# Kernel tuning notes

Measured on AMD Instinct MI355X. Metric: run time of the kernel, lower is better.

The kernel has to match this reference:

```python
import jax, jax.numpy as jnp
import numpy as np

HIDDEN = 1024
NUM_HEADS = 16
HEAD_DIM = HIDDEN // NUM_HEADS


def setup_inputs() -> dict:
    key = jax.random.key(0)
    k1, k2, k3 = jax.random.split(key, 3)
    x = jax.random.normal(k1, (2, 2048, HIDDEN), dtype=jnp.float32)
    # Linear weights, torch layout [out_features, in_features]
    w_qkv = jax.random.normal(k2, (3 * HIDDEN, HIDDEN), dtype=jnp.float32) * 0.02
    w_out = jax.random.normal(k3, (HIDDEN, HIDDEN), dtype=jnp.float32) * 0.02
    return {"x": x, "w_qkv": w_qkv, "w_out": w_out}


def reference(x, w_qkv, w_out):
    B, S, H = x.shape
    scale = 1.0 / HEAD_DIM ** 0.5
    qkv = jnp.einsum('bsh,oh->bso', x, w_qkv)              # [B,S,3H]
    qkv = qkv.reshape(B, S, 3, NUM_HEADS, HEAD_DIM)
    qkv = jnp.transpose(qkv, (2, 0, 3, 1, 4))               # [3,B,nh,S,hd]
    q, k, v = qkv[0], qkv[1], qkv[2]
    scores = jnp.einsum('bnsd,bntd->bnst', q, k) * scale    # [B,nh,S,S]
    attn = jax.nn.softmax(scores, axis=-1)
    out = jnp.einsum('bnst,bntd->bnsd', attn, v)            # [B,nh,S,hd]
    out = jnp.transpose(out, (0, 2, 1, 3)).reshape(B, S, H)
    return jnp.einsum('bsh,oh->bso', out, w_out)
```

## Files before the change

### kernel.cpp

```cpp
#include <hip/hip_runtime.h>
#include <stdint.h>

typedef unsigned short u16;
typedef __bf16 bf16x8 __attribute__((ext_vector_type(8)));
typedef float f32x4 __attribute__((ext_vector_type(4)));
typedef float f32x16 __attribute__((ext_vector_type(16)));
typedef unsigned u32x4 __attribute__((ext_vector_type(4)));

#define DEVI __device__ __forceinline__

typedef __attribute__((address_space(1))) void gvoid;
typedef __attribute__((address_space(3))) void lvoid;

DEVI u16 f2b(float f) {
  unsigned x = __builtin_bit_cast(unsigned, f);
  return (u16)((x + 0x7fffu + ((x >> 16) & 1u)) >> 16);
}

DEVI float exp2g(float x) { return __builtin_amdgcn_exp2f(x); }

DEVI void gload_lds16(const void* g, void* l) {
  __builtin_amdgcn_global_load_lds((gvoid*)g, (lvoid*)l, 16, 0, 0);
}

#define QSCALE 0.18033688011112042f

__global__ void cast_all(const float* __restrict__ x, const float* __restrict__ wqkv,
                         const float* __restrict__ wout, u16* __restrict__ outb) {
  int i = blockIdx.x * 256 + threadIdx.x;
  int stride = gridDim.x * 256;
  for (; i < 2097152; i += stride) {
    const float* src;
    float sc = 1.0f;
    if (i < 1048576) {
      src = x + 4 * (long)i;
    } else if (i < 1835008) {
      int j = i - 1048576;
      src = wqkv + 4 * (long)j;
      if (j < 262144) sc = QSCALE;
    } else {
      src = wout + 4 * (long)(i - 1835008);
    }
    float4 v = *(const float4*)src;
    ushort4 o;
    o.x = f2b(v.x * sc); o.y = f2b(v.y * sc); o.z = f2b(v.z * sc); o.w = f2b(v.w * sc);
    ((ushort4*)outb)[i] = o;
  }
}

__global__ __launch_bounds__(512, 2)
void gemm_qkv(const u16* __restrict__ A, const u16* __restrict__ B,
              u16* __restrict__ qk, u16* __restrict__ vT, int K) {
  __shared__ u16 SA[2][256 * 64];
  __shared__ u16 SB[2][256 * 64];
  const int tid = threadIdx.x;
  const int lane = tid & 63;
  const int lr = lane & 15;
  const int lg = lane >> 4;
  const int wid = tid >> 6;
  const int wm = wid >> 2;
  const int wn = wid & 3;
  const long bm = (long)blockIdx.y * 256;
  const long bn = (long)blockIdx.x * 256;
  const int wr = wm * 128;
  const int wc = wn * 64;

  f32x4 acc[8][4];
#pragma unroll
  for (int i = 0; i < 8; ++i)
#pragma unroll
    for (int j = 0; j < 4; ++j)
      acc[i][j] = (f32x4){0.f, 0.f, 0.f, 0.f};

  int srow[4], scol[4], sdst[4];
#pragma unroll
  for (int q = 0; q < 4; ++q) {
    int b = tid + q * 512;
    srow[q] = b >> 3;
    scol[q] = ((b & 7) ^ ((b >> 3) & 7)) * 8;
    sdst[q] = b * 16;
  }

  auto stage = [&](int buf, int k0) {
#pragma unroll
    for (int q = 0; q < 4; ++q)
      gload_lds16(A + (bm + srow[q]) * (long)K + k0 + scol[q], (char*)SA[buf] + sdst[q]);
#pragma unroll
    for (int q = 0; q < 4; ++q)
      gload_lds16(B + (bn + srow[q]) * (long)K + k0 + scol[q], (char*)SB[buf] + sdst[q]);
  };

  stage(0, 0);
  asm volatile("s_waitcnt vmcnt(0)" ::: "memory");
  __builtin_amdgcn_s_barrier();
  __builtin_amdgcn_sched_barrier(0);

  const int NITER = K >> 6;
  for (int it = 0; it < NITER; ++it) {
    const int cur = it & 1;
    if (it + 1 < NITER) stage(cur ^ 1, (it + 1) * 64);

    const char* cA = (const char*)SA[cur];
    const char* cB = (const char*)SB[cur];

    bf16x8 bf[4][2];
#pragma unroll
    for (int ni = 0; ni < 4; ++ni)
#pragma unroll
      for (int kk = 0; kk < 2; ++kk) {
        int row = wc + ni * 16 + lr;
        bf[ni][kk] = *(const bf16x8*)(cB + row * 128 + (((kk * 4 + lg) ^ (row & 7)) << 4));
      }

#pragma unroll
    for (int half = 0; half < 2; ++half) {
      bf16x8 af[4][2];
#pragma unroll
      for (int mi = 0; mi < 4; ++mi)
#pragma unroll
        for (int kk = 0; kk < 2; ++kk) {
          int row = wr + half * 64 + mi * 16 + lr;
          af[mi][kk] = *(const bf16x8*)(cA + row * 128 + (((kk * 4 + lg) ^ (row & 7)) << 4));
        }
      __builtin_amdgcn_s_setprio(1);
#pragma unroll
      for (int mi = 0; mi < 4; ++mi)
#pragma unroll
        for (int ni = 0; ni < 4; ++ni)
#pragma unroll
          for (int kk = 0; kk < 2; ++kk)
            acc[half * 4 + mi][ni] =
                __builtin_amdgcn_mfma_f32_16x16x32_bf16(af[mi][kk], bf[ni][kk], acc[half * 4 + mi][ni], 0, 0, 0);
      __builtin_amdgcn_s_setprio(0);
    }

    if (it + 1 < NITER) {
      asm volatile("s_waitcnt vmcnt(0)" ::: "memory");
      __builtin_amdgcn_s_barrier();
      __builtin_amdgcn_sched_barrier(0);
    }
  }

  if (bn >= 2048) {
#pragma unroll
    for (int mi = 0; mi < 8; ++mi)
#pragma unroll
      for (int ni = 0; ni < 4; ++ni) {
        long tok = bm + wr + mi * 16 + lg * 4;
        long f = bn + wc + ni * 16 + lr - 2048;
        ushort4 st;
        st.x = f2b(acc[mi][ni][0]);
        st.y = f2b(acc[mi][ni][1]);
        st.z = f2b(acc[mi][ni][2]);
        st.w = f2b(acc[mi][ni][3]);
        u16* dst = vT + (((tok >> 11) << 4) + (f >> 6)) * 131072 + (f & 63) * 2048 + (tok & 2047);
        *(ushort4*)dst = st;
      }
  } else {
#pragma unroll
    for (int mi = 0; mi < 8; ++mi)
#pragma unroll
      for (int ni = 0; ni < 4; ++ni)
#pragma unroll
        for (int r = 0; r < 4; ++r) {
          long row = bm + wr + mi * 16 + lg * 4 + r;
          long col = bn + wc + ni * 16 + lr;
          qk[row * 2048 + col] = f2b(acc[mi][ni][r]);
        }
  }
}

template<int OUT, int TM, int SWZ>
__global__ __launch_bounds__(256)
void gemm_bt(const u16* __restrict__ A, const u16* __restrict__ B, void* __restrict__ Cv,
             void* __restrict__ Cv2, int M, int N, int K) {
  constexpr int MI = TM / 32;
  __shared__ u16 lA[TM * 64];
  __shared__ u16 lB[128 * 64];
  const int tid = threadIdx.x;
  const int lane = tid & 63;
  const int lr = lane & 15;
  const int lg = lane >> 4;
  const int wid = tid >> 6;

  long bm, bn;
  if (SWZ) {
    const int f = blockIdx.x + gridDim.x * blockIdx.y;
    const int chunk = (gridDim.x * gridDim.y) >> 3;
    const int ln = (f & 7) * chunk + (f >> 3);
    bm = (long)(ln % gridDim.y) * TM;
    bn = (long)(ln / gridDim.y) * 128;
  } else {
    bm = (long)blockIdx.y * TM;
    bn = (long)blockIdx.x * 128;
  }

  const int wr = (wid >> 1) * (TM / 2);
  const int wc = (wid & 1) * 64;

  f32x4 acc[MI][4];
#pragma unroll
  for (int i = 0; i < MI; ++i)
#pragma unroll
    for (int j = 0; j < 4; ++j)
      acc[i][j] = (f32x4){0.f, 0.f, 0.f, 0.f};

  for (int k0 = 0; k0 < K; k0 += 64) {
#pragma unroll
    for (int q = 0; q < MI; ++q) {
      int bi = tid + q * 256;
      int row = bi >> 3;
      int col = ((bi & 7) ^ (row & 7)) * 8;
      gload_lds16(A + (bm + row) * (long)K + k0 + col, (char*)lA + bi * 16);
    }
#pragma unroll
    for (int q = 0; q < 4; ++q) {
      int bi = tid + q * 256;
      int row = bi >> 3;
      int col = ((bi & 7) ^ (row & 7)) * 8;
      gload_lds16(B + (bn + row) * (long)K + k0 + col, (char*)lB + bi * 16);
    }
    __syncthreads();
#pragma unroll
    for (int kk = 0; kk < 2; ++kk) {
      bf16x8 af[MI], bfr[4];
      int kb = kk * 4 + lg;
#pragma unroll
      for (int mi = 0; mi < MI; ++mi) {
        int row = wr + mi * 16 + lr;
        af[mi] = *(const bf16x8*)((const char*)lA + row * 128 + ((kb ^ (row & 7)) << 4));
      }
#pragma unroll
      for (int ni = 0; ni < 4; ++ni) {
        int row = wc + ni * 16 + lr;
        bfr[ni] = *(const bf16x8*)((const char*)lB + row * 128 + ((kb ^ (row & 7)) << 4));
      }
#pragma unroll
      for (int mi = 0; mi < MI; ++mi)
#pragma unroll
        for (int ni = 0; ni < 4; ++ni)
          acc[mi][ni] = __builtin_amdgcn_mfma_f32_16x16x32_bf16(af[mi], bfr[ni], acc[mi][ni], 0, 0, 0);
    }
    __syncthreads();
  }

  const long strideN = (OUT == 2) ? 2048 : N;
#pragma unroll
  for (int mi = 0; mi < MI; ++mi)
#pragma unroll
    for (int ni = 0; ni < 4; ++ni)
#pragma unroll
      for (int r = 0; r < 4; ++r) {
        long row = bm + wr + mi * 16 + lg * 4 + r;
        long col = bn + wc + ni * 16 + lr;
        float v = acc[mi][ni][r];
        if (OUT == 1) ((float*)Cv)[row * strideN + col] = v;
        else          ((u16*)Cv)[row * strideN + col] = f2b(v);
      }
}

__global__ __launch_bounds__(256, 2)
void attn_fwd(const u16* __restrict__ qk, const u16* __restrict__ vT,
              u16* __restrict__ outb) {
  __shared__ char SM[33280];

  const int tid = threadIdx.x;
  const int lane = tid & 63;
  const int wid = tid >> 6;
  const int ql = lane & 31;
  const int h  = lane >> 5;
  const int th = wid >> 1;
  const int qw = wid & 1;

  const int flat = blockIdx.x + (blockIdx.y << 4) + (blockIdx.z << 8);
  const int swz  = ((flat & 7) << 6) + (flat >> 3);
  const int qt = swz & 15;
  const int hd = (swz >> 4) & 15;
  const int b  = swz >> 8;

  const long rowbase = (long)b * 2048;
  const int qcol = hd * 64;
  const int kcol = 1024 + hd * 64;
  const int TSK = 64 * 2048;
  const long vhb = ((long)b * 16 + hd) * 131072;

  const int q0w = qt * 128 + qw * 64;
  bf16x8 qfA[4], qfB[4];
  {
    const u16* qpA = qk + (rowbase + q0w + ql) * 2048 + qcol + h * 8;
    const u16* qpB = qpA + 32 * 2048;
#pragma unroll
    for (int dblk = 0; dblk < 4; ++dblk) {
      qfA[dblk] = *(const bf16x8*)(qpA + dblk * 16);
      qfB[dblk] = *(const bf16x8*)(qpB + dblk * 16);
    }
  }

  float lA = 0.f, lB = 0.f;
  f32x16 oA[2], oB[2];
#pragma unroll
  for (int d = 0; d < 2; ++d)
#pragma unroll
    for (int r = 0; r < 16; ++r) { oA[d][r] = 0.f; oB[d][r] = 0.f; }

  const int c0 = tid, c1 = tid + 256;
  const int rk0 = c0 >> 3, ck0 = ((c0 & 7) ^ (rk0 & 7)) * 8;
  const int rk1 = c1 >> 3, ck1 = ((c1 & 7) ^ (rk1 & 7)) * 8;
  const int d0 = c0 * 16, d1 = c1 * 16;
  const u16* kp0 = qk + (rowbase + rk0) * 2048 + kcol + ck0;
  const u16* kp1 = qk + (rowbase + rk1) * 2048 + kcol + ck1;
  const u16* vp0 = vT + vhb + rk0 * 2048 + ck0;
  const u16* vp1 = vT + vhb + rk1 * 2048 + ck1;

  gload_lds16(kp0, SM + d0);          gload_lds16(kp1, SM + d1);
  gload_lds16(vp0, SM + 16384 + d0);  gload_lds16(vp1, SM + 16384 + d1);
  kp0 += TSK; kp1 += TSK; vp0 += 64; vp1 += 64;
  asm volatile("s_waitcnt vmcnt(0)" ::: "memory");
  __builtin_amdgcn_s_barrier();
  __builtin_amdgcn_sched_barrier(0);

  for (int tt = 0; tt < 16; ++tt) {
#pragma unroll
    for (int P = 0; P < 2; ++P) {
      char* KsCur = SM + P * 8192;
      char* VsCur = SM + 16384 + P * 8192;
      char* KsNxt = SM + (P ^ 1) * 8192;
      char* VsNxt = SM + 16384 + (P ^ 1) * 8192;

      gload_lds16(kp0, KsNxt + d0);  gload_lds16(kp1, KsNxt + d1);
      gload_lds16(vp0, VsNxt + d0);  gload_lds16(vp1, VsNxt + d1);
      kp0 += TSK; kp1 += TSK; vp0 += 64; vp1 += 64;

      f32x16 sA, sB;
#pragma unroll
      for (int r = 0; r < 16; ++r) { sA[r] = 0.f; sB[r] = 0.f; }
      const char* Kb = KsCur + (th * 32 + ql) * 128;
      __builtin_amdgcn_s_setprio(1);
#pragma unroll
      for (int kd = 0; kd < 4; ++kd) {
        bf16x8 kf = *(const bf16x8*)(Kb + (((kd * 2 + h) ^ (ql & 7)) << 4));
        sA = __builtin_amdgcn_mfma_f32_32x32x16_bf16(kf, qfA[kd], sA, 0, 0, 0);
        sB = __builtin_amdgcn_mfma_f32_32x32x16_bf16(kf, qfB[kd], sB, 0, 0, 0);
      }
      __builtin_amdgcn_s_setprio(0);

#pragma unroll
      for (int r = 0; r < 16; ++r) sA[r] = exp2g(sA[r]);
#pragma unroll
      for (int r = 0; r < 16; ++r) sB[r] = exp2g(sB[r]);
      lA += (((sA[0] + sA[1]) + (sA[2] + sA[3])) + ((sA[4] + sA[5]) + (sA[6] + sA[7])))
          + (((sA[8] + sA[9]) + (sA[10] + sA[11])) + ((sA[12] + sA[13]) + (sA[14] + sA[15])));
      lB += (((sB[0] + sB[1]) + (sB[2] + sB[3])) + ((sB[4] + sB[5]) + (sB[6] + sB[7])))
          + (((sB[8] + sB[9]) + (sB[10] + sB[11])) + ((sB[12] + sB[13]) + (sB[14] + sB[15])));

      unsigned wA[8], wB[8];
#pragma unroll
      for (int m = 0; m < 8; ++m) {
        asm("v_cvt_pk_bf16_f32 %0, %1, %2" : "=v"(wA[m]) : "v"(sA[2 * m]), "v"(sA[2 * m + 1]));
        asm("v_cvt_pk_bf16_f32 %0, %1, %2" : "=v"(wB[m]) : "v"(sB[2 * m]), "v"(sB[2 * m + 1]));
      }

      bf16x8 pbA[2], pbB[2];
#pragma unroll
      for (int ks = 0; ks < 2; ++ks) {
        unsigned a0 = wA[4 * ks],     a2 = wA[4 * ks + 2];
        unsigned a1 = wA[4 * ks + 1], a3 = wA[4 * ks + 3];
        asm("s_nop 1\n\tv_permlane32_swap_b32 %0, %1" : "+v"(a0), "+v"(a2));
        asm("s_nop 1\n\tv_permlane32_swap_b32 %0, %1" : "+v"(a1), "+v"(a3));
        u32x4 t; t[0] = a0; t[1] = a1; t[2] = a2; t[3] = a3;
        pbA[ks] = __builtin_bit_cast(bf16x8, t);
        unsigned b0 = wB[4 * ks],     b2 = wB[4 * ks + 2];
        unsigned b1 = wB[4 * ks + 1], b3 = wB[4 * ks + 3];
        asm("s_nop 1\n\tv_permlane32_swap_b32 %0, %1" : "+v"(b0), "+v"(b2));
        asm("s_nop 1\n\tv_permlane32_swap_b32 %0, %1" : "+v"(b1), "+v"(b3));
        u32x4 u; u[0] = b0; u[1] = b1; u[2] = b2; u[3] = b3;
        pbB[ks] = __builtin_bit_cast(bf16x8, u);
      }

      __builtin_amdgcn_s_setprio(1);
#pragma unroll
      for (int dblk = 0; dblk < 2; ++dblk) {
        const char* Vb = VsCur + (dblk * 32 + ql) * 128;
#pragma unroll
        for (int ks = 0; ks < 2; ++ks) {
          bf16x8 vf = *(const bf16x8*)(Vb + (((th * 4 + ks * 2 + h) ^ (ql & 7)) << 4));
          oA[dblk] = __builtin_amdgcn_mfma_f32_32x32x16_bf16(vf, pbA[ks], oA[dblk], 0, 0, 0);
          oB[dblk] = __builtin_amdgcn_mfma_f32_32x32x16_bf16(vf, pbB[ks], oB[dblk], 0, 0, 0);
        }
      }
      __builtin_amdgcn_s_setprio(0);

      asm volatile("s_waitcnt vmcnt(0)" ::: "memory");
      __builtin_amdgcn_s_barrier();
      __builtin_amdgcn_sched_barrier(0);
    }
  }
  __syncthreads();

  float pxA = lA, pyA = lA;
  asm("s_nop 1\n\tv_permlane32_swap_b32 %0, %1" : "+v"(pxA), "+v"(pyA));
  float lwA = lA + (h ? pxA : pyA);
  float pxB = lB, pyB = lB;
  asm("s_nop 1\n\tv_permlane32_swap_b32 %0, %1" : "+v"(pxB), "+v"(pyB));
  float lwB = lB + (h ? pxB : pyB);

  if (th == 1) {
    char* regA = SM + (qw * 2 + 0) * 8192;
    char* regB = SM + (qw * 2 + 1) * 8192;
#pragma unroll
    for (int dblk = 0; dblk < 2; ++dblk)
#pragma unroll
      for (int r = 0; r < 16; ++r) {
        int dl = dblk * 32 + (r & 3) + 8 * (r >> 2) + 4 * h;
        *(float*)(regA + dl * 128 + ql * 4) = oA[dblk][r];
        *(float*)(regB + dl * 128 + ql * 4) = oB[dblk][r];
      }
    if (h == 0) {
      *(float*)(SM + 32768 + (qw * 2 + 0) * 128 + ql * 4) = lwA;
      *(float*)(SM + 32768 + (qw * 2 + 1) * 128 + ql * 4) = lwB;
    }
  }
  __syncthreads();
  if (th == 0) {
    const char* regA = SM + (qw * 2 + 0) * 8192;
    const char* regB = SM + (qw * 2 + 1) * 8192;
#pragma unroll
    for (int dblk = 0; dblk < 2; ++dblk)
#pragma unroll
      for (int r = 0; r < 16; ++r) {
        int dl = dblk * 32 + (r & 3) + 8 * (r >> 2) + 4 * h;
        oA[dblk][r] += *(const float*)(regA + dl * 128 + ql * 4);
        oB[dblk][r] += *(const float*)(regB + dl * 128 + ql * 4);
      }
    float invA = 1.0f / (lwA + *(const float*)(SM + 32768 + (qw * 2 + 0) * 128 + ql * 4));
    float invB = 1.0f / (lwB + *(const float*)(SM + 32768 + (qw * 2 + 1) * 128 + ql * 4));
    long rowA = rowbase + q0w + ql;
    long rowB = rowA + 32;
#pragma unroll
    for (int dblk = 0; dblk < 2; ++dblk)
#pragma unroll
      for (int m = 0; m < 4; ++m) {
        ushort4 stA;
        stA.x = f2b(oA[dblk][4 * m + 0] * invA);
        stA.y = f2b(oA[dblk][4 * m + 1] * invA);
        stA.z = f2b(oA[dblk][4 * m + 2] * invA);
        stA.w = f2b(oA[dblk][4 * m + 3] * invA);
        *(ushort4*)(outb + rowA * 1024 + qcol + dblk * 32 + 8 * m + 4 * h) = stA;
        ushort4 stB;
        stB.x = f2b(oB[dblk][4 * m + 0] * invB);
        stB.y = f2b(oB[dblk][4 * m + 1] * invB);
        stB.z = f2b(oB[dblk][4 * m + 2] * invB);
        stB.w = f2b(oB[dblk][4 * m + 3] * invB);
        *(ushort4*)(outb + rowB * 1024 + qcol + dblk * 32 + 8 * m + 4 * h) = stB;
      }
  }
}

extern "C" void kernel_launch(void* const* d_in, const int* in_sizes, int n_in,
                              void* d_out, int out_size, void* d_ws, size_t ws_size,
                              hipStream_t stream) {
  const float* x     = (const float*)d_in[0];
  const float* w_qkv = (const float*)d_in[1];
  const float* w_out = (const float*)d_in[2];
  float* out = (float*)d_out;

  char* ws = (char*)d_ws;
  u16* xb    = (u16*)(ws);
  u16* wqkvb = (u16*)(ws + 8388608);
  u16* woutb = (u16*)(ws + 14680064);
  u16* qk    = (u16*)(ws + 16777216);
  u16* vT    = (u16*)(ws + 33554432);
  u16* attn  = (u16*)(ws + 41943040);

  cast_all<<<2048, 256, 0, stream>>>(x, w_qkv, w_out, xb);

  gemm_qkv<<<dim3(12, 16), 512, 0, stream>>>(xb, wqkvb, qk, vT, 1024);

  attn_fwd<<<dim3(16, 16, 2), 256, 0, stream>>>(qk, vT, attn);

  gemm_bt<1, 64, 0><<<dim3(8, 64), 256, 0, stream>>>(attn, woutb, out, nullptr, 4096, 1024, 1024);
}
```

Measured before the change: 111.4 us.

## Restructure QKV GEMM into four-phase pipelined loop with split A/B prefetch

Rewrites the QKV projection GEMM main loop so each K-step is split into four quarter-tile MFMA phases. Each phase interleaves LDS fragment reads, a partial global-to-LDS prefetch of the next A or B half-tile, and barriers, with a vmcnt(4) wait instead of a full drain. The aim is to overlap global loads with MFMA work and cut the per-iteration stall on memory. K is hardcoded to 1024, and the unused template options of the output GEMM are removed. The change adds many more barriers per iteration and relies on careful buffer reuse of the A slot while other waves may still read it.

```diff
diff --git a/kernel.cpp b/kernel.cpp
--- a/kernel.cpp
+++ b/kernel.cpp
@@ -22,6 +22,9 @@
 DEVI void gload_lds16(const void* g, void* l) {
   __builtin_amdgcn_global_load_lds((gvoid*)g, (lvoid*)l, 16, 0, 0);
 }
+
+#define BARRIER() do { asm volatile("" ::: "memory"); __builtin_amdgcn_s_barrier(); __builtin_amdgcn_sched_barrier(0); } while (0)
+#define LGKM0()   do { asm volatile("s_waitcnt lgkmcnt(0)" ::: "memory"); __builtin_amdgcn_sched_barrier(0); } while (0)
 
 #define QSCALE 0.18033688011112042f
 
@@ -50,9 +53,8 @@
 
 __global__ __launch_bounds__(512, 2)
 void gemm_qkv(const u16* __restrict__ A, const u16* __restrict__ B,
-              u16* __restrict__ qk, u16* __restrict__ vT, int K) {
-  __shared__ u16 SA[2][256 * 64];
-  __shared__ u16 SB[2][256 * 64];
+              u16* __restrict__ qk, u16* __restrict__ vT) {
+  __shared__ char SM[131072];
   const int tid = threadIdx.x;
   const int lane = tid & 63;
   const int lr = lane & 15;
@@ -62,85 +64,137 @@
   const int wn = wid & 3;
   const long bm = (long)blockIdx.y * 256;
   const long bn = (long)blockIdx.x * 256;
+
+  const int r0 = tid >> 3;
+  const int c0 = ((tid & 7) ^ (r0 & 7)) * 8;
+  const int dst0 = tid * 16;
+  const u16* tA = A + (bm + r0) * 1024 + c0;
+  const u16* tB = B + (bn + r0) * 1024 + c0;
+
+#define STAGE_A(buf, h, ko) do { \
+    gload_lds16(tA + (h) * 131072 + (ko),         SM + (buf) * 32768 + (h) * 16384 + dst0); \
+    gload_lds16(tA + (h) * 131072 + (ko) + 65536, SM + (buf) * 32768 + (h) * 16384 + dst0 + 8192); } while (0)
+#define STAGE_B(buf, h, ko) do { \
+    gload_lds16(tB + (h) * 131072 + (ko),         SM + 65536 + (buf) * 32768 + (h) * 16384 + dst0); \
+    gload_lds16(tB + (h) * 131072 + (ko) + 65536, SM + 65536 + (buf) * 32768 + (h) * 16384 + dst0 + 8192); } while (0)
+
+  f32x4 acc[8][4];
+#pragma unroll
+  for (int i = 0; i < 8; ++i)
+#pragma unroll
+    for (int j = 0; j < 4; ++j)
+      acc[i][j] = (f32x4){0.f, 0.f, 0.f, 0.f};
+
+  const int wmo = wm * 16384;
+  const int bho = (wn >> 1) * 16384;
+  const int bro = (wn & 1) * 64;
+
+  STAGE_A(0, 0, 0);  STAGE_A(0, 1, 0);
+  STAGE_B(0, 0, 0);  STAGE_B(0, 1, 0);
+  STAGE_A(1, 0, 64); STAGE_A(1, 1, 64);
+
+  for (int T = 0; T < 16; ++T) {
+    const int pb = T & 1;
+    const int koB = (T + 1) * 64;
+    const int koA = (T + 2) * 64;
+    const char* LA = SM + pb * 32768 + wmo;
+    const char* LB = SM + 65536 + pb * 32768 + bho;
+
+    asm volatile("s_waitcnt vmcnt(4)" ::: "memory");
+    __builtin_amdgcn_s_barrier();
+    __builtin_amdgcn_sched_barrier(0);
+
+    bf16x8 a0[4][2], a1[4][2], bfr[2][2];
+
+#pragma unroll
+    for (int mi = 0; mi < 4; ++mi)
+#pragma unroll
+      for (int kk = 0; kk < 2; ++kk) {
+        int r = mi * 16 + lr;
+        a0[mi][kk] = *(const bf16x8*)(LA + r * 128 + (((kk * 4 + lg) ^ (r & 7)) << 4));
+      }
+#pragma unroll
+    for (int ni = 0; ni < 2; ++ni)
+#pragma unroll
+      for (int kk = 0; kk < 2; ++kk) {
+        int r = bro + ni * 16 + lr;
+        bfr[ni][kk] = *(const bf16x8*)(LB + r * 128 + (((kk * 4 + lg) ^ (r & 7)) << 4));
+      }
+    STAGE_B(pb ^ 1, 0, koB);
+    BARRIER();
+    LGKM0();
+    __builtin_amdgcn_s_setprio(1);
+#pragma unroll
+    for (int mi = 0; mi < 4; ++mi)
+#pragma unroll
+      for (int ni = 0; ni < 2; ++ni)
+#pragma unroll
+        for (int kk = 0; kk < 2; ++kk)
+          acc[mi][ni] = __builtin_amdgcn_mfma_f32_16x16x32_bf16(a0[mi][kk], bfr[ni][kk], acc[mi][ni], 0, 0, 0);
+    __builtin_amdgcn_s_setprio(0);
+    BARRIER();
+
+#pragma unroll
+    for (int mi = 0; mi < 4; ++mi)
+#pragma unroll
+      for (int kk = 0; kk < 2; ++kk) {
+        int r = (mi + 4) * 16 + lr;
+        a1[mi][kk] = *(const bf16x8*)(LA + r * 128 + (((kk * 4 + lg) ^ (r & 7)) << 4));
+      }
+    STAGE_B(pb ^ 1, 1, koB);
+    BARRIER();
+    LGKM0();
+    __builtin_amdgcn_s_setprio(1);
+#pragma unroll
+    for (int mi = 0; mi < 4; ++mi)
+#pragma unroll
+      for (int ni = 0; ni < 2; ++ni)
+#pragma unroll
+        for (int kk = 0; kk < 2; ++kk)
+          acc[4 + mi][ni] = __builtin_amdgcn_mfma_f32_16x16x32_bf16(a1[mi][kk], bfr[ni][kk], acc[4 + mi][ni], 0, 0, 0);
+    __builtin_amdgcn_s_setprio(0);
+    BARRIER();
+
+#pragma unroll
+    for (int ni = 0; ni < 2; ++ni)
+#pragma unroll
+      for (int kk = 0; kk < 2; ++kk) {
+        int r = bro + (ni + 2) * 16 + lr;
+        bfr[ni][kk] = *(const bf16x8*)(LB + r * 128 + (((kk * 4 + lg) ^ (r & 7)) << 4));
+      }
+    STAGE_A(pb, 0, koA);
+    BARRIER();
+    LGKM0();
+    __builtin_amdgcn_s_setprio(1);
+#pragma unroll
+    for (int mi = 0; mi < 4; ++mi)
+#pragma unroll
+      for (int ni = 0; ni < 2; ++ni)
+#pragma unroll
+        for (int kk = 0; kk < 2; ++kk)
+          acc[mi][2 + ni] = __builtin_amdgcn_mfma_f32_16x16x32_bf16(a0[mi][kk], bfr[ni][kk], acc[mi][2 + ni], 0, 0, 0);
+    __builtin_amdgcn_s_setprio(0);
+    BARRIER();
+
+    STAGE_A(pb, 1, koA);
+    BARRIER();
+    LGKM0();
+    __builtin_amdgcn_s_setprio(1);
+#pragma unroll
+    for (int mi = 0; mi < 4; ++mi)
+#pragma unroll
+      for (int ni = 0; ni < 2; ++ni)
+#pragma unroll
+        for (int kk = 0; kk < 2; ++kk)
+          acc[4 + mi][2 + ni] = __builtin_amdgcn_mfma_f32_16x16x32_bf16(a1[mi][kk], bfr[ni][kk], acc[4 + mi][2 + ni], 0, 0, 0);
+    __builtin_amdgcn_s_setprio(0);
+    BARRIER();
+  }
+
+  asm volatile("s_waitcnt vmcnt(0)" ::: "memory");
+
   const int wr = wm * 128;
   const int wc = wn * 64;
-
-  f32x4 acc[8][4];
-#pragma unroll
-  for (int i = 0; i < 8; ++i)
-#pragma unroll
-    for (int j = 0; j < 4; ++j)
-      acc[i][j] = (f32x4){0.f, 0.f, 0.f, 0.f};
-
-  int srow[4], scol[4], sdst[4];
-#pragma unroll
-  for (int q = 0; q < 4; ++q) {
-    int b = tid + q * 512;
-    srow[q] = b >> 3;
-    scol[q] = ((b & 7) ^ ((b >> 3) & 7)) * 8;
-    sdst[q] = b * 16;
-  }
-
-  auto stage = [&](int buf, int k0) {
-#pragma unroll
-    for (int q = 0; q < 4; ++q)
-      gload_lds16(A + (bm + srow[q]) * (long)K + k0 + scol[q], (char*)SA[buf] + sdst[q]);
-#pragma unroll
-    for (int q = 0; q < 4; ++q)
-      gload_lds16(B + (bn + srow[q]) * (long)K + k0 + scol[q], (char*)SB[buf] + sdst[q]);
-  };
-
-  stage(0, 0);
-  asm volatile("s_waitcnt vmcnt(0)" ::: "memory");
-  __builtin_amdgcn_s_barrier();
-  __builtin_amdgcn_sched_barrier(0);
-
-  const int NITER = K >> 6;
-  for (int it = 0; it < NITER; ++it) {
-    const int cur = it & 1;
-    if (it + 1 < NITER) stage(cur ^ 1, (it + 1) * 64);
-
-    const char* cA = (const char*)SA[cur];
-    const char* cB = (const char*)SB[cur];
-
-    bf16x8 bf[4][2];
-#pragma unroll
-    for (int ni = 0; ni < 4; ++ni)
-#pragma unroll
-      for (int kk = 0; kk < 2; ++kk) {
-        int row = wc + ni * 16 + lr;
-        bf[ni][kk] = *(const bf16x8*)(cB + row * 128 + (((kk * 4 + lg) ^ (row & 7)) << 4));
-      }
-
-#pragma unroll
-    for (int half = 0; half < 2; ++half) {
-      bf16x8 af[4][2];
-#pragma unroll
-      for (int mi = 0; mi < 4; ++mi)
-#pragma unroll
-        for (int kk = 0; kk < 2; ++kk) {
-          int row = wr + half * 64 + mi * 16 + lr;
-          af[mi][kk] = *(const bf16x8*)(cA + row * 128 + (((kk * 4 + lg) ^ (row & 7)) << 4));
-        }
-      __builtin_amdgcn_s_setprio(1);
-#pragma unroll
-      for (int mi = 0; mi < 4; ++mi)
-#pragma unroll
-        for (int ni = 0; ni < 4; ++ni)
-#pragma unroll
-          for (int kk = 0; kk < 2; ++kk)
-            acc[half * 4 + mi][ni] =
-                __builtin_amdgcn_mfma_f32_16x16x32_bf16(af[mi][kk], bf[ni][kk], acc[half * 4 + mi][ni], 0, 0, 0);
-      __builtin_amdgcn_s_setprio(0);
-    }
-
-    if (it + 1 < NITER) {
-      asm volatile("s_waitcnt vmcnt(0)" ::: "memory");
-      __builtin_amdgcn_s_barrier();
-      __builtin_amdgcn_sched_barrier(0);
-    }
-  }
-
   if (bn >= 2048) {
 #pragma unroll
     for (int mi = 0; mi < 8; ++mi)
@@ -168,12 +222,14 @@
           qk[row * 2048 + col] = f2b(acc[mi][ni][r]);
         }
   }
-}
-
-template<int OUT, int TM, int SWZ>
+#undef STAGE_A
+#undef STAGE_B
+}
+
+template<int TM>
 __global__ __launch_bounds__(256)
-void gemm_bt(const u16* __restrict__ A, const u16* __restrict__ B, void* __restrict__ Cv,
-             void* __restrict__ Cv2, int M, int N, int K) {
+void gemm_out(const u16* __restrict__ A, const u16* __restrict__ B, float* __restrict__ Cv,
+              int M, int N, int K) {
   constexpr int MI = TM / 32;
   __shared__ u16 lA[TM * 64];
   __shared__ u16 lB[128 * 64];
@@ -182,19 +238,8 @@
   const int lr = lane & 15;
   const int lg = lane >> 4;
   const int wid = tid >> 6;
-
-  long bm, bn;
-  if (SWZ) {
-    const int f = blockIdx.x + gridDim.x * blockIdx.y;
-    const int chunk = (gridDim.x * gridDim.y) >> 3;
-    const int ln = (f & 7) * chunk + (f >> 3);
-    bm = (long)(ln % gridDim.y) * TM;
-    bn = (long)(ln / gridDim.y) * 128;
-  } else {
-    bm = (long)blockIdx.y * TM;
-    bn = (long)blockIdx.x * 128;
-  }
-
+  const long bm = (long)blockIdx.y * TM;
+  const long bn = (long)blockIdx.x * 128;
   const int wr = (wid >> 1) * (TM / 2);
   const int wc = (wid & 1) * 64;
 
@@ -243,8 +288,6 @@
     }
     __syncthreads();
   }
-
-  const long strideN = (OUT == 2) ? 2048 : N;
 #pragma unroll
   for (int mi = 0; mi < MI; ++mi)
 #pragma unroll
@@ -253,9 +296,7 @@
       for (int r = 0; r < 4; ++r) {
         long row = bm + wr + mi * 16 + lg * 4 + r;
         long col = bn + wc + ni * 16 + lr;
-        float v = acc[mi][ni][r];
-        if (OUT == 1) ((float*)Cv)[row * strideN + col] = v;
-        else          ((u16*)Cv)[row * strideN + col] = f2b(v);
+        Cv[row * (long)N + col] = acc[mi][ni][r];
       }
 }
 
@@ -474,9 +515,9 @@
 
   cast_all<<<2048, 256, 0, stream>>>(x, w_qkv, w_out, xb);
 
-  gemm_qkv<<<dim3(12, 16), 512, 0, stream>>>(xb, wqkvb, qk, vT, 1024);
+  gemm_qkv<<<dim3(12, 16), 512, 0, stream>>>(xb, wqkvb, qk, vT);
 
   attn_fwd<<<dim3(16, 16, 2), 256, 0, stream>>>(qk, vT, attn);
 
-  gemm_bt<1, 64, 0><<<dim3(8, 64), 256, 0, stream>>>(attn, woutb, out, nullptr, 4096, 1024, 1024);
-}
+  gemm_out<64><<<dim3(8, 64), 256, 0, stream>>>(attn, woutb, out, 4096, 1024, 1024);
+}
```

Result: faster. 107.0 us (-4.0%).
